# Kernel tuning notes

Hardware: AMD Instinct MI355X
Metric: run time of the kernel (lower is better)

The kernel has to match this reference:

```python
import jax, jax.numpy as jnp
import numpy as np

B, L = 16, 2048
D_MODEL, N_LAYERS, D_STATE, D_CONV, EXPAND, N_CLASSES = 64, 4, 16, 4, 2, 35
D_INNER = EXPAND * D_MODEL
DT_RANK = (D_MODEL + 15) // 16  # ceil(d_model/16) = 4


def setup_inputs() -> dict:
    key = jax.random.key(0)
    ks = jax.random.split(key, 16)
    s = 0.02
    A_log = jnp.log(jnp.tile(jnp.arange(1, D_STATE + 1, dtype=jnp.float32), (D_INNER, 1)))  # mamba S4D-real init
    inp = {
        "x": jax.random.normal(ks[0], (B, L), jnp.float32),
        "W_proj": jax.random.normal(ks[1], (D_MODEL, 1), jnp.float32) * s,
        "b_proj": jnp.zeros((D_MODEL,), jnp.float32),
        "ln_g": jnp.ones((N_LAYERS, D_MODEL), jnp.float32),
        "ln_b": jnp.zeros((N_LAYERS, D_MODEL), jnp.float32),
        "W_in": jax.random.normal(ks[2], (N_LAYERS, 2 * D_INNER, D_MODEL), jnp.float32) * s,
        "conv_w": jax.random.normal(ks[3], (N_LAYERS, D_INNER, D_CONV), jnp.float32) * s,
        "conv_b": jnp.zeros((N_LAYERS, D_INNER), jnp.float32),
        "W_x": jax.random.normal(ks[4], (N_LAYERS, DT_RANK + 2 * D_STATE, D_INNER), jnp.float32) * s,
        "W_dt": jax.random.normal(ks[5], (N_LAYERS, D_INNER, DT_RANK), jnp.float32) * s,
        "b_dt": jax.random.normal(ks[6], (N_LAYERS, D_INNER), jnp.float32) * s,
        "A_log": jnp.tile(A_log[None], (N_LAYERS, 1, 1)),
        "Dp": jnp.ones((N_LAYERS, D_INNER), jnp.float32),
        "W_out": jax.random.normal(ks[7], (N_LAYERS, D_MODEL, D_INNER), jnp.float32) * s,
        "W_head": jax.random.normal(ks[8], (N_CLASSES, D_MODEL), jnp.float32) * s,
        "b_head": jnp.zeros((N_CLASSES,), jnp.float32),
    }
    return inp


def _layernorm(x, g, b, eps=1e-5):
    mu = x.mean(-1, keepdims=True)
    var = ((x - mu) ** 2).mean(-1, keepdims=True)
    return (x - mu) * jax.lax.rsqrt(var + eps) * g + b


def _mamba(x, W_in, conv_w, conv_b, W_x, W_dt, b_dt, A_log, Dp, W_out):
    # x: [B, L, d_model]
    d_inner = W_in.shape[0] // 2
    d_state = A_log.shape[-1]
    dt_rank = W_dt.shape[1]
    xz = jnp.einsum('bld,ed->ble', x, W_in)          # [B,L,2*d_inner]
    u, z = jnp.split(xz, 2, axis=-1)
    # causal depthwise conv1d (torch conv with padding=d_conv-1 then [..., :L])
    uc = jax.lax.conv_general_dilated(
        u.transpose(0, 2, 1), conv_w[:, None, :], (1,), [(conv_w.shape[-1] - 1, 0)],
        dimension_numbers=('NCH', 'OIH', 'NCH'), feature_group_count=d_inner,
    ).transpose(0, 2, 1) + conv_b
    u = jax.nn.silu(uc)                               # [B,L,d_inner]
    x_dbl = jnp.einsum('ble,re->blr', u, W_x)
    dt = x_dbl[..., :dt_rank]
    Bm = x_dbl[..., dt_rank:dt_rank + d_state]
    Cm = x_dbl[..., dt_rank + d_state:]
    delta = jax.nn.softplus(jnp.einsum('blr,er->ble', dt, W_dt) + b_dt)  # [B,L,d_inner]
    A = -jnp.exp(A_log)                               # [d_inner, d_state]

    def step(h, inputs):
        d_t, u_t, B_t, C_t = inputs                   # [B,e],[B,e],[B,n],[B,n]
        h = jnp.exp(d_t[..., None] * A) * h + (d_t * u_t)[..., None] * B_t[:, None, :]
        y = jnp.einsum('ben,bn->be', h, C_t)
        return h, y

    h0 = jnp.zeros((x.shape[0], d_inner, d_state), x.dtype)
    xs = (delta.transpose(1, 0, 2), u.transpose(1, 0, 2),
          Bm.transpose(1, 0, 2), Cm.transpose(1, 0, 2))
    _, ys = jax.lax.scan(step, h0, xs)                # ys: [L,B,d_inner]
    y = ys.transpose(1, 0, 2) + u * Dp
    y = y * jax.nn.silu(z)
    return jnp.einsum('ble,de->bld', y, W_out)


def reference(x, W_proj, b_proj, ln_g, ln_b, W_in, conv_w, conv_b, W_x, W_dt,
              b_dt, A_log, Dp, W_out, W_head, b_head):
    # projection: Linear(1, d_model) on x.unsqueeze(-1)
    h = x[..., None] * W_proj[:, 0] + b_proj          # [B,L,d_model]
    n_layers = ln_g.shape[0]
    for i in range(n_layers):
        h = h + _mamba(_layernorm(h, ln_g[i], ln_b[i]), W_in[i], conv_w[i],
                       conv_b[i], W_x[i], W_dt[i], b_dt[i], A_log[i], Dp[i], W_out[i])
    h = h.mean(axis=1)                                # [B,d_model]
    return h @ W_head.T + b_head                      # [B,n_classes]
```

## Files before the change

### kernel.cpp

```cpp
#include <hip/hip_runtime.h>
#include <math.h>

#define B_   16
#define L_   2048
#define DMOD 64
#define E_   128
#define S_   16
#define NLAY 4
#define NCLS 35
#define NC   16
#define CL   128

#define DPPADD(x, ctrl) \
  x += __int_as_float(__builtin_amdgcn_update_dpp(0, __float_as_int(x), ctrl, 0xf, 0xf, true))

__global__ void k_init(const float* __restrict__ x, const float* __restrict__ Wp,
                       const float* __restrict__ bp, float* __restrict__ h,
                       float* __restrict__ mean) {
  int i = blockIdx.x * 256 + threadIdx.x;
  if (i < B_ * DMOD) mean[i] = 0.f;
  int d = i & 63;
  int r = i >> 6;
  h[i] = x[r] * Wp[d] + bp[d];
}

__global__ __launch_bounds__(256) void k_lnxz(
    const float* __restrict__ h, const float* __restrict__ lgm,
    const float* __restrict__ lbt, const float* __restrict__ W,
    float* __restrict__ xz) {
  __shared__ float xl[32 * 68];
  int tid = threadIdx.x;
  int row = tid >> 3, j = tid & 7;
  size_t gr = (size_t)blockIdx.x * 32 + row;
  const float4* hp = (const float4*)(h + gr * 64 + j * 8);
  float4 v0 = hp[0], v1 = hp[1];
  float s = v0.x + v0.y + v0.z + v0.w + v1.x + v1.y + v1.z + v1.w;
  s += __shfl_xor(s, 1, 8); s += __shfl_xor(s, 2, 8); s += __shfl_xor(s, 4, 8);
  float mu = s * (1.f / 64.f);
  float d0, q = 0.f;
  d0 = v0.x - mu; q += d0 * d0;  d0 = v0.y - mu; q += d0 * d0;
  d0 = v0.z - mu; q += d0 * d0;  d0 = v0.w - mu; q += d0 * d0;
  d0 = v1.x - mu; q += d0 * d0;  d0 = v1.y - mu; q += d0 * d0;
  d0 = v1.z - mu; q += d0 * d0;  d0 = v1.w - mu; q += d0 * d0;
  q += __shfl_xor(q, 1, 8); q += __shfl_xor(q, 2, 8); q += __shfl_xor(q, 4, 8);
  float rs = rsqrtf(q * (1.f / 64.f) + 1e-5f);
  const float4* gp = (const float4*)(lgm + j * 8);
  const float4* bp2 = (const float4*)(lbt + j * 8);
  float4 g0 = gp[0], g1 = gp[1], b0 = bp2[0], b1 = bp2[1];
  float* xw = &xl[row * 68 + j * 8];
  xw[0] = (v0.x - mu) * rs * g0.x + b0.x;
  xw[1] = (v0.y - mu) * rs * g0.y + b0.y;
  xw[2] = (v0.z - mu) * rs * g0.z + b0.z;
  xw[3] = (v0.w - mu) * rs * g0.w + b0.w;
  xw[4] = (v1.x - mu) * rs * g1.x + b1.x;
  xw[5] = (v1.y - mu) * rs * g1.y + b1.y;
  xw[6] = (v1.z - mu) * rs * g1.z + b1.z;
  xw[7] = (v1.w - mu) * rs * g1.w + b1.w;
  __syncthreads();

  int e = tid;
  float acc[32];
#pragma unroll
  for (int r2 = 0; r2 < 32; r2++) acc[r2] = 0.f;
  const float4* Wv = (const float4*)(W + e * 64);
#pragma unroll
  for (int k = 0; k < 16; k++) {
    float4 w = Wv[k];
#pragma unroll
    for (int r2 = 0; r2 < 32; r2++) {
      const float4 xv = *(const float4*)&xl[r2 * 68 + k * 4];
      acc[r2] = fmaf(w.x, xv.x, fmaf(w.y, xv.y, fmaf(w.z, xv.z, fmaf(w.w, xv.w, acc[r2]))));
    }
  }
  float* xo = xz + (size_t)blockIdx.x * 32 * 256 + e;
#pragma unroll
  for (int r2 = 0; r2 < 32; r2++) xo[r2 * 256] = acc[r2];
}

__global__ __launch_bounds__(256) void k_conv_xdbl(
    const float* __restrict__ xz, const float* __restrict__ cw,
    const float* __restrict__ cb, const float* __restrict__ Wx,
    const float* __restrict__ Wdt, const float* __restrict__ bdt,
    float* __restrict__ us, float* __restrict__ dadb, float* __restrict__ bc) {
  __shared__ float Wxl[36 * 132];
  __shared__ float usl[8 * 132];
  __shared__ float uh[11 * 128];
  __shared__ float xdl[8 * 8];
  int tid = threadIdx.x;
  int b = blockIdx.x >> 8;
  int l0 = (blockIdx.x & 255) * 8;

  for (int i = tid; i < 36 * 128; i += 256)
    Wxl[(i >> 7) * 132 + (i & 127)] = Wx[i];
  for (int i = tid; i < 11 * 128; i += 256) {
    int rr = i >> 7, e2 = i & 127;
    int gl = l0 + rr - 3;
    uh[i] = (gl >= 0) ? xz[((size_t)(b * L_ + gl)) * 256 + e2] : 0.f;
  }
  __syncthreads();

  int e = tid & 127, sub = tid >> 7;
  const float4 cwv = *(const float4*)(cw + e * 4);
  float cbv = cb[e];
#pragma unroll
  for (int rr = 0; rr < 4; rr++) {
    int row = sub * 4 + rr;
    float uc = cbv + uh[row * 128 + e] * cwv.x + uh[(row + 1) * 128 + e] * cwv.y
             + uh[(row + 2) * 128 + e] * cwv.z + uh[(row + 3) * 128 + e] * cwv.w;
    float sg = 1.f / (1.f + __expf(-uc));
    float uv = uc * sg;
    usl[row * 132 + e] = uv;
    us[((size_t)(b * L_ + l0 + row)) * 128 + e] = uv;
  }
  __syncthreads();

  for (int o = tid; o < 288; o += 256) {
    int row = o / 36;
    int r = o - row * 36;
    const float* up = &usl[row * 132];
    const float* wp = &Wxl[r * 132];
    int rot = (r & 1) << 2;
    float a0 = 0.f, a1 = 0.f, a2 = 0.f, a3 = 0.f;
#pragma unroll
    for (int i = 0; i < 32; i++) {
      int c = (i + rot) & 31;
      float4 u4 = *(const float4*)(up + c * 4);
      float4 w4 = *(const float4*)(wp + c * 4);
      a0 = fmaf(u4.x, w4.x, a0); a1 = fmaf(u4.y, w4.y, a1);
      a2 = fmaf(u4.z, w4.z, a2); a3 = fmaf(u4.w, w4.w, a3);
    }
    float acc = (a0 + a1) + (a2 + a3);
    int l = l0 + row;
    if (r < 4)        xdl[row * 8 + r] = acc;
    else if (r < 20)  bc[(((size_t)(b * L_ + l)) * 16 + (r - 4)) * 2] = acc;
    else              bc[(((size_t)(b * L_ + l)) * 16 + (r - 20)) * 2 + 1] = acc;
  }
  __syncthreads();

  const float4 wdt = *(const float4*)(Wdt + e * 4);
  float bd = bdt[e];
  float2* dadb2 = (float2*)dadb;
#pragma unroll
  for (int rr = 0; rr < 4; rr++) {
    int row = sub * 4 + rr;
    float pre = bd + xdl[row * 8 + 0] * wdt.x + xdl[row * 8 + 1] * wdt.y
              + xdl[row * 8 + 2] * wdt.z + xdl[row * 8 + 3] * wdt.w;
    float ex = __expf(pre);
    float sp = (pre > 20.f) ? pre : __logf(1.f + ex);
    float uv = usl[row * 132 + e];
    dadb2[((size_t)(b * L_ + l0 + row)) * 128 + e] = make_float2(sp, sp * uv);
  }
}

__global__ __launch_bounds__(256) void k_scan1(
    const float* __restrict__ dadb, const float* __restrict__ bc,
    const float* __restrict__ Alog, float2* __restrict__ PE) {
  int tid = threadIdx.x;
  int g = tid >> 4, n = tid & 15;
  int b = blockIdx.x >> 7;
  int eg = (blockIdx.x >> 4) & 7;
  int c = blockIdx.x & 15;
  int e = eg * 16 + g;
  float A2 = -__expf(Alog[e * 16 + n]) * 1.44269504088896f;
  const float2* dp = (const float2*)dadb + (size_t)(b * L_ + c * CL) * 128 + e;
  const float2* bp = (const float2*)bc + (size_t)(b * L_ + c * CL) * 16 + n;
  float P = 1.f, hst = 0.f;
  for (int t0 = 0; t0 < CL; t0 += 8) {
#pragma unroll
    for (int k = 0; k < 8; k++) {
      float2 dd = dp[(size_t)(t0 + k) * 128];
      float2 cv = bp[(size_t)(t0 + k) * 16];
      float a = exp2f(dd.x * A2);
      P *= a;
      hst = fmaf(a, hst, dd.y * cv.x);
    }
  }
  PE[(size_t)c * 32768 + ((blockIdx.x >> 4) << 8) + tid] = make_float2(P, hst);
}

__global__ __launch_bounds__(256) void k_scan2(const float2* __restrict__ PE,
                                               float* __restrict__ HS) {
  int i = blockIdx.x * 256 + threadIdx.x;
  float H = 0.f;
#pragma unroll
  for (int c = 0; c < NC; c++) {
    float2 pe = PE[(size_t)c * 32768 + i];
    HS[(size_t)c * 32768 + i] = H;
    H = fmaf(pe.x, H, pe.y);
  }
}

__global__ __launch_bounds__(256) void k_scan3(
    const float* __restrict__ dadb, const float* __restrict__ bc,
    const float* __restrict__ Alog, const float* __restrict__ HS,
    float* __restrict__ ys) {
  int tid = threadIdx.x;
  int g = tid >> 4, n = tid & 15;
  int b = blockIdx.x >> 7;
  int eg = (blockIdx.x >> 4) & 7;
  int c = blockIdx.x & 15;
  int e = eg * 16 + g;
  float A2 = -__expf(Alog[e * 16 + n]) * 1.44269504088896f;
  const float2* dp = (const float2*)dadb + (size_t)(b * L_ + c * CL) * 128 + e;
  const float2* bp = (const float2*)bc + (size_t)(b * L_ + c * CL) * 16 + n;
  float* yp = ys + (size_t)(b * L_ + c * CL) * 256 + e;
  float hst = HS[(size_t)c * 32768 + ((blockIdx.x >> 4) << 8) + tid];
  for (int t0 = 0; t0 < CL; t0 += 16) {
    float yv[16];
#pragma unroll
    for (int k = 0; k < 16; k++) {
      float2 dd = dp[(size_t)(t0 + k) * 128];
      float2 cv = bp[(size_t)(t0 + k) * 16];
      float a = exp2f(dd.x * A2);
      hst = fmaf(a, hst, dd.y * cv.x);
      float p = hst * cv.y;
      DPPADD(p, 0x111);
      DPPADD(p, 0x112);
      DPPADD(p, 0x114);
      DPPADD(p, 0x118);
      yv[k] = p;
    }
    if (n == 15) {
#pragma unroll
      for (int k = 0; k < 16; k++) yp[(size_t)(t0 + k) * 256] = yv[k];
    }
  }
}

__global__ __launch_bounds__(256) void k_out(
    const float* __restrict__ xz, const float* __restrict__ us,
    const float* __restrict__ Dp, const float* __restrict__ W,
    float* __restrict__ h) {
  __shared__ float yl[64 * 132];
  int tid = threadIdx.x;
  size_t r0 = (size_t)blockIdx.x * 64;
  for (int i = tid; i < 64 * 128; i += 256) {
    int row = i >> 7, e = i & 127;
    size_t gr = r0 + row;
    float yv = xz[gr * 256 + e];
    float uv = us[gr * 128 + e];
    float z  = xz[gr * 256 + 128 + e];
    float sg = 1.f / (1.f + __expf(-z));
    yl[row * 132 + e] = (yv + uv * Dp[e]) * z * sg;
  }
  __syncthreads();
  int c = tid & 63, rg = tid >> 6;
  float acc[16];
#pragma unroll
  for (int r = 0; r < 16; r++) acc[r] = 0.f;
  const float4* Wv = (const float4*)(W + c * 128);
#pragma unroll
  for (int k = 0; k < 32; k++) {
    float4 w = Wv[k];
#pragma unroll
    for (int r = 0; r < 16; r++) {
      float4 yv = *(const float4*)&yl[(rg * 16 + r) * 132 + k * 4];
      acc[r] = fmaf(w.x, yv.x, fmaf(w.y, yv.y, fmaf(w.z, yv.z, fmaf(w.w, yv.w, acc[r]))));
    }
  }
#pragma unroll
  for (int r = 0; r < 16; r++) {
    size_t idx = (r0 + rg * 16 + r) * 64 + c;
    h[idx] += acc[r];
  }
}

__global__ void k_mean(const float* __restrict__ h, float* __restrict__ mean) {
  int b = blockIdx.x >> 5, lc = blockIdx.x & 31;
  int d = threadIdx.x;
  const float* p = h + ((size_t)(b * L_ + lc * 64)) * 64 + d;
  float s = 0.f;
#pragma unroll 8
  for (int i = 0; i < 64; i++) s += p[i * 64];
  atomicAdd(mean + b * 64 + d, s * (1.f / 2048.f));
}

__global__ void k_head(const float* __restrict__ mean, const float* __restrict__ Wh,
                       const float* __restrict__ bh, float* __restrict__ out) {
  int i = threadIdx.x;
  if (i >= B_ * NCLS) return;
  int b = i / NCLS, c = i - b * NCLS;
  const float* m = mean + b * 64;
  const float* w = Wh + c * 64;
  float acc = bh[c];
#pragma unroll
  for (int d = 0; d < 64; d++) acc = fmaf(m[d], w[d], acc);
  out[i] = acc;
}

extern "C" void kernel_launch(void* const* d_in, const int* in_sizes, int n_in,
                              void* d_out, int out_size, void* d_ws, size_t ws_size,
                              hipStream_t stream) {
  const float* x     = (const float*)d_in[0];
  const float* Wp    = (const float*)d_in[1];
  const float* bp    = (const float*)d_in[2];
  const float* lng   = (const float*)d_in[3];
  const float* lnb   = (const float*)d_in[4];
  const float* Win   = (const float*)d_in[5];
  const float* cw    = (const float*)d_in[6];
  const float* cb    = (const float*)d_in[7];
  const float* Wx    = (const float*)d_in[8];
  const float* Wdt   = (const float*)d_in[9];
  const float* bdt   = (const float*)d_in[10];
  const float* Alog  = (const float*)d_in[11];
  const float* Dp    = (const float*)d_in[12];
  const float* Wout  = (const float*)d_in[13];
  const float* Whead = (const float*)d_in[14];
  const float* bhead = (const float*)d_in[15];
  float* out = (float*)d_out;
  float* w = (float*)d_ws;

  float* h    = w;
  float* xz   = w + 2097152;
  float* us   = w + 10485760;
  float* dadb = w + 14680064;
  float* bc   = w + 23068672;
  float* mean = w + 24117248;
  float2* PE  = (float2*)(w + 24118272);
  float* HS   = w + 25166848;

  k_init<<<8192, 256, 0, stream>>>(x, Wp, bp, h, mean);
  for (int l = 0; l < NLAY; l++) {
    k_lnxz<<<1024, 256, 0, stream>>>(h, lng + l * 64, lnb + l * 64,
                                     Win + l * 256 * 64, xz);
    k_conv_xdbl<<<4096, 256, 0, stream>>>(xz, cw + l * 128 * 4, cb + l * 128,
                                          Wx + l * 36 * 128, Wdt + l * 128 * 4,
                                          bdt + l * 128, us, dadb, bc);
    k_scan1<<<2048, 256, 0, stream>>>(dadb, bc, Alog + l * 128 * 16, PE);
    k_scan2<<<128, 256, 0, stream>>>(PE, HS);
    k_scan3<<<2048, 256, 0, stream>>>(dadb, bc, Alog + l * 128 * 16, HS, xz);
    k_out<<<512, 256, 0, stream>>>(xz, us, Dp + l * 128, Wout + l * 64 * 128, h);
  }
  k_mean<<<512, 64, 0, stream>>>(h, mean);
  k_head<<<1, 576, 0, stream>>>(mean, Whead, bhead, out);
}
```

Before: 914.1 us.

## Interleave two independent scan chunks per thread and replace product with exp-of-sum

Each thread in the chunked scan kernels now processes two independent chunks (c and c+8) at once, halving the grid. The two recurrences are interleaved to raise instruction-level parallelism and hide the latency of the serial FMA chain, and loads are batched ahead of the compute. In scan1 the running product of decays is replaced by summing deltas and taking one exp2 at the end, which saves a multiply per step and may change rounding slightly. Fewer blocks lowers occupancy and wave count, and register use grows, so launch bounds were added to keep 4 blocks per CU.

After: 920.4 us. Within noise of the previous version (+0.7%).

```diff
diff --git a/kernel.cpp b/kernel.cpp
--- a/kernel.cpp
+++ b/kernel.cpp
@@ -152,30 +152,41 @@
   }
 }
 
-__global__ __launch_bounds__(256) void k_scan1(
+__global__ __launch_bounds__(256, 4) void k_scan1(
     const float* __restrict__ dadb, const float* __restrict__ bc,
     const float* __restrict__ Alog, float2* __restrict__ PE) {
   int tid = threadIdx.x;
   int g = tid >> 4, n = tid & 15;
-  int b = blockIdx.x >> 7;
-  int eg = (blockIdx.x >> 4) & 7;
-  int c = blockIdx.x & 15;
+  int b  = blockIdx.x >> 6;
+  int eg = (blockIdx.x >> 3) & 7;
+  int cp = blockIdx.x & 7;
   int e = eg * 16 + g;
   float A2 = -__expf(Alog[e * 16 + n]) * 1.44269504088896f;
-  const float2* dp = (const float2*)dadb + (size_t)(b * L_ + c * CL) * 128 + e;
-  const float2* bp = (const float2*)bc + (size_t)(b * L_ + c * CL) * 16 + n;
-  float P = 1.f, hst = 0.f;
-  for (int t0 = 0; t0 < CL; t0 += 8) {
-#pragma unroll
-    for (int k = 0; k < 8; k++) {
-      float2 dd = dp[(size_t)(t0 + k) * 128];
-      float2 cv = bp[(size_t)(t0 + k) * 16];
-      float a = exp2f(dd.x * A2);
-      P *= a;
-      hst = fmaf(a, hst, dd.y * cv.x);
-    }
-  }
-  PE[(size_t)c * 32768 + ((blockIdx.x >> 4) << 8) + tid] = make_float2(P, hst);
+  const float2* dp0 = (const float2*)dadb + (size_t)(b * L_ + cp * CL) * 128 + e;
+  const float2* bp0 = (const float2*)bc   + (size_t)(b * L_ + cp * CL) * 16  + n;
+  const float2* dp1 = dp0 + (size_t)8 * CL * 128;
+  const float2* bp1 = bp0 + (size_t)8 * CL * 16;
+  float S0 = 0.f, h0 = 0.f, S1 = 0.f, h1 = 0.f;
+  for (int t0 = 0; t0 < CL; t0 += 4) {
+    float2 d0[4], c0[4], d1[4], c1[4];
+#pragma unroll
+    for (int k = 0; k < 4; k++) {
+      d0[k] = dp0[(t0 + k) * 128]; c0[k] = bp0[(t0 + k) * 16];
+      d1[k] = dp1[(t0 + k) * 128]; c1[k] = bp1[(t0 + k) * 16];
+    }
+#pragma unroll
+    for (int k = 0; k < 4; k++) {
+      S0 += d0[k].x;
+      float a0 = exp2f(d0[k].x * A2);
+      h0 = fmaf(a0, h0, d0[k].y * c0[k].x);
+      S1 += d1[k].x;
+      float a1 = exp2f(d1[k].x * A2);
+      h1 = fmaf(a1, h1, d1[k].y * c1[k].x);
+    }
+  }
+  size_t base = ((size_t)(b * 8 + eg) << 8) + tid;
+  PE[(size_t)cp * 32768 + base]       = make_float2(exp2f(S0 * A2), h0);
+  PE[(size_t)(cp + 8) * 32768 + base] = make_float2(exp2f(S1 * A2), h1);
 }
 
 __global__ __launch_bounds__(256) void k_scan2(const float2* __restrict__ PE,
@@ -190,39 +201,53 @@
   }
 }
 
-__global__ __launch_bounds__(256) void k_scan3(
+__global__ __launch_bounds__(256, 4) void k_scan3(
     const float* __restrict__ dadb, const float* __restrict__ bc,
     const float* __restrict__ Alog, const float* __restrict__ HS,
     float* __restrict__ ys) {
   int tid = threadIdx.x;
   int g = tid >> 4, n = tid & 15;
-  int b = blockIdx.x >> 7;
-  int eg = (blockIdx.x >> 4) & 7;
-  int c = blockIdx.x & 15;
+  int b  = blockIdx.x >> 6;
+  int eg = (blockIdx.x >> 3) & 7;
+  int cp = blockIdx.x & 7;
   int e = eg * 16 + g;
   float A2 = -__expf(Alog[e * 16 + n]) * 1.44269504088896f;
-  const float2* dp = (const float2*)dadb + (size_t)(b * L_ + c * CL) * 128 + e;
-  const float2* bp = (const float2*)bc + (size_t)(b * L_ + c * CL) * 16 + n;
-  float* yp = ys + (size_t)(b * L_ + c * CL) * 256 + e;
-  float hst = HS[(size_t)c * 32768 + ((blockIdx.x >> 4) << 8) + tid];
-  for (int t0 = 0; t0 < CL; t0 += 16) {
-    float yv[16];
-#pragma unroll
-    for (int k = 0; k < 16; k++) {
-      float2 dd = dp[(size_t)(t0 + k) * 128];
-      float2 cv = bp[(size_t)(t0 + k) * 16];
-      float a = exp2f(dd.x * A2);
-      hst = fmaf(a, hst, dd.y * cv.x);
-      float p = hst * cv.y;
-      DPPADD(p, 0x111);
-      DPPADD(p, 0x112);
-      DPPADD(p, 0x114);
-      DPPADD(p, 0x118);
-      yv[k] = p;
+  const float2* dp0 = (const float2*)dadb + (size_t)(b * L_ + cp * CL) * 128 + e;
+  const float2* bp0 = (const float2*)bc   + (size_t)(b * L_ + cp * CL) * 16  + n;
+  const float2* dp1 = dp0 + (size_t)8 * CL * 128;
+  const float2* bp1 = bp0 + (size_t)8 * CL * 16;
+  float* yp0 = ys + (size_t)(b * L_ + cp * CL) * 256 + e;
+  float* yp1 = yp0 + (size_t)8 * CL * 256;
+  size_t base = ((size_t)(b * 8 + eg) << 8) + tid;
+  float h0 = HS[(size_t)cp * 32768 + base];
+  float h1 = HS[(size_t)(cp + 8) * 32768 + base];
+  for (int t0 = 0; t0 < CL; t0 += 4) {
+    float2 d0[4], c0[4], d1[4], c1[4];
+#pragma unroll
+    for (int k = 0; k < 4; k++) {
+      d0[k] = dp0[(t0 + k) * 128]; c0[k] = bp0[(t0 + k) * 16];
+      d1[k] = dp1[(t0 + k) * 128]; c1[k] = bp1[(t0 + k) * 16];
+    }
+    float y0[4], y1[4];
+#pragma unroll
+    for (int k = 0; k < 4; k++) {
+      float a0 = exp2f(d0[k].x * A2);
+      h0 = fmaf(a0, h0, d0[k].y * c0[k].x);
+      float p0 = h0 * c0[k].y;
+      DPPADD(p0, 0x111); DPPADD(p0, 0x112); DPPADD(p0, 0x114); DPPADD(p0, 0x118);
+      y0[k] = p0;
+      float a1 = exp2f(d1[k].x * A2);
+      h1 = fmaf(a1, h1, d1[k].y * c1[k].x);
+      float p1 = h1 * c1[k].y;
+      DPPADD(p1, 0x111); DPPADD(p1, 0x112); DPPADD(p1, 0x114); DPPADD(p1, 0x118);
+      y1[k] = p1;
     }
     if (n == 15) {
 #pragma unroll
-      for (int k = 0; k < 16; k++) yp[(size_t)(t0 + k) * 256] = yv[k];
+      for (int k = 0; k < 4; k++) {
+        yp0[(t0 + k) * 256] = y0[k];
+        yp1[(t0 + k) * 256] = y1[k];
+      }
     }
   }
 }
@@ -326,9 +351,9 @@
     k_conv_xdbl<<<4096, 256, 0, stream>>>(xz, cw + l * 128 * 4, cb + l * 128,
                                           Wx + l * 36 * 128, Wdt + l * 128 * 4,
                                           bdt + l * 128, us, dadb, bc);
-    k_scan1<<<2048, 256, 0, stream>>>(dadb, bc, Alog + l * 128 * 16, PE);
+    k_scan1<<<1024, 256, 0, stream>>>(dadb, bc, Alog + l * 128 * 16, PE);
     k_scan2<<<128, 256, 0, stream>>>(PE, HS);
-    k_scan3<<<2048, 256, 0, stream>>>(dadb, bc, Alog + l * 128 * 16, HS, xz);
+    k_scan3<<<1024, 256, 0, stream>>>(dadb, bc, Alog + l * 128 * 16, HS, xz);
     k_out<<<512, 256, 0, stream>>>(xz, us, Dp + l * 128, Wout + l * 64 * 128, h);
   }
   k_mean<<<512, 64, 0, stream>>>(h, mean);
```
